# Kernel optimization log

Measured on AMD Instinct MI355X. Metric: run time of the kernel, lower is better.

Reference implementation:

```python
import jax, jax.numpy as jnp
import numpy as np

B, L = 16, 65536
NUM_BINS = 256
H = 64


def setup_inputs() -> dict:
    key = jax.random.key(0)
    k1, k2, k3, k4 = jax.random.split(key, 4)
    x = jax.random.normal(k1, (B, L), dtype=jnp.float32)
    mask = jax.random.uniform(k4, (B, L)) < 0.1
    x = jnp.where(mask, jnp.nan, x)
    # monotonically increasing bin edges
    bins = jnp.sort(jax.random.normal(k2, (NUM_BINS,), dtype=jnp.float32) * 1.5)
    # nn.Embedding(num_bins + 1, H), default init N(0,1); row 0 is the mask token
    emb_table = jax.random.normal(k3, (NUM_BINS + 1, H), dtype=jnp.float32)
    return {"x": x, "bins": bins, "emb_table": emb_table}


def reference(x, bins, emb_table):
    # BinEmbedding.bin with left_closed=True:
    #   idx = clamp(argmin([x>=b for b in bins] ++ [0]) - 1, min=0)
    # which equals clamp(count(bins <= x) - 1, min=0) = clamp(searchsorted(right) - 1, 0).
    # NaN inputs compare False everywhere in torch -> argmin=0 -> idx=0, then the
    # forward re-injects NaN and DiscreteEmbedding maps NaN -> token 0 (mask).
    nans = jnp.isnan(x)
    xs = jnp.where(nans, jnp.float32(0.0), x)  # sanitize for searchsorted
    idx = jnp.maximum(jnp.searchsorted(bins, xs, side="right") - 1, 0)  # (B, L)
    tok = jnp.where(nans, 0, idx + 1)  # +1 shift; 0 reserved for mask token
    return emb_table[tok]  # (B, L, H)
```

## Files before the change

kernel.cpp:

```cpp
#include <hip/hip_runtime.h>
#include <stdint.h>

#define N_POS (16 * 65536)
#define NBINS 256
#define HDIM  64


typedef float vfloat4 __attribute__((ext_vector_type(4)));

#define THREADS        256
#define POS_PER_TILE   256
#define TILES          8
#define POS_PER_BLOCK  (POS_PER_TILE * TILES)
#define NBLOCKS        (N_POS / POS_PER_BLOCK)
#define EMB_ROWS       (NBINS + 1)
#define EMB_CHUNKS     (EMB_ROWS * 16)

__global__ __launch_bounds__(THREADS, 2)
void BinEmbedding_49520972923592_kernel(
    const float* __restrict__ x,
    const float* __restrict__ bins,
    const vfloat4* __restrict__ embv,
    vfloat4* __restrict__ out)
{
    __shared__ vfloat4 s_emb[EMB_CHUNKS];
    __shared__ float   s_bins[NBINS];
    __shared__ int     s_tok[2][POS_PER_TILE];

    const int tid = threadIdx.x;

    s_bins[tid] = bins[tid];
    for (int c = tid; c < EMB_CHUNKS; c += THREADS)
        s_emb[c] = embv[c];

    const long pbase = (long)blockIdx.x * POS_PER_BLOCK;
    float xv = x[pbase + tid];
    __syncthreads();

    for (int tile = 0; tile < TILES; ++tile) {
        int cnt = 0;
#pragma unroll
        for (int step = 128; step >= 1; step >>= 1) {
            const int cand = cnt + step;
            cnt = (s_bins[cand - 1] <= xv) ? cand : cnt;
        }
        cnt += (s_bins[NBINS - 1] <= xv) ? 1 : 0;

        s_tok[tile & 1][tid] = (xv != xv) ? 0 : (cnt > 0 ? cnt : 1);

        if (tile + 1 < TILES)
            xv = x[pbase + (tile + 1) * POS_PER_TILE + tid];

        __syncthreads();

        const int* st = s_tok[tile & 1];
        const long cbase = (pbase + (long)tile * POS_PER_TILE) * 16;
#pragma unroll
        for (int i = 0; i < 16; ++i) {
            const int l = i * THREADS + tid;
            out[cbase + l] = s_emb[st[l >> 4] * 16 + (l & 15)];
        }
    }
}

extern "C" void kernel_launch(void* const* d_in, const int* in_sizes, int n_in,
                              void* d_out, int out_size, void* d_ws, size_t ws_size,
                              hipStream_t stream) {
    const float*   x    = (const float*)d_in[0];
    const float*   bins = (const float*)d_in[1];
    const vfloat4* emb  = (const vfloat4*)d_in[2];
    vfloat4* out = (vfloat4*)d_out;

    const dim3 grid(NBLOCKS), block(THREADS);
    hipLaunchKernelGGL(BinEmbedding_49520972923592_kernel, grid, block, 0, stream,
                       x, bins, emb, out);
}
```

Measured before the change: 271.9 us.

## Batch binary searches across all positions per thread before a single store phase

```diff
diff --git a/kernel.cpp b/kernel.cpp
--- a/kernel.cpp
+++ b/kernel.cpp
@@ -9,10 +9,10 @@
 typedef float vfloat4 __attribute__((ext_vector_type(4)));
 
 #define THREADS        256
-#define POS_PER_TILE   256
-#define TILES          8
-#define POS_PER_BLOCK  (POS_PER_TILE * TILES)
+#define POS_PER_TH     8
+#define POS_PER_BLOCK  (THREADS * POS_PER_TH)
 #define NBLOCKS        (N_POS / POS_PER_BLOCK)
+#define CHUNKS_PER_BLOCK (POS_PER_BLOCK * 16)
 #define EMB_ROWS       (NBINS + 1)
 #define EMB_CHUNKS     (EMB_ROWS * 16)
 
@@ -25,41 +25,49 @@
 {
     __shared__ vfloat4 s_emb[EMB_CHUNKS];
     __shared__ float   s_bins[NBINS];
-    __shared__ int     s_tok[2][POS_PER_TILE];
+    __shared__ int     s_tok[POS_PER_BLOCK];
 
     const int tid = threadIdx.x;
+    const long pbase = (long)blockIdx.x * POS_PER_BLOCK;
 
     s_bins[tid] = bins[tid];
-    for (int c = tid; c < EMB_CHUNKS; c += THREADS)
-        s_emb[c] = embv[c];
+#pragma unroll
+    for (int c = tid, k = 0; k < EMB_CHUNKS / THREADS + 1; ++k, c += THREADS)
+        if (c < EMB_CHUNKS) s_emb[c] = embv[c];
 
-    const long pbase = (long)blockIdx.x * POS_PER_BLOCK;
-    float xv = x[pbase + tid];
+    float xv[POS_PER_TH];
+#pragma unroll
+    for (int j = 0; j < POS_PER_TH; ++j)
+        xv[j] = x[pbase + j * THREADS + tid];
+
     __syncthreads();
 
-    for (int tile = 0; tile < TILES; ++tile) {
-        int cnt = 0;
+    int cnt[POS_PER_TH];
 #pragma unroll
-        for (int step = 128; step >= 1; step >>= 1) {
-            const int cand = cnt + step;
-            cnt = (s_bins[cand - 1] <= xv) ? cand : cnt;
+    for (int j = 0; j < POS_PER_TH; ++j) cnt[j] = 0;
+#pragma unroll
+    for (int step = 128; step >= 1; step >>= 1) {
+#pragma unroll
+        for (int j = 0; j < POS_PER_TH; ++j) {
+            const int cand = cnt[j] + step;
+            cnt[j] = (s_bins[cand - 1] <= xv[j]) ? cand : cnt[j];
         }
-        cnt += (s_bins[NBINS - 1] <= xv) ? 1 : 0;
+    }
+#pragma unroll
+    for (int j = 0; j < POS_PER_TH; ++j) {
+        const int c = cnt[j] + ((s_bins[NBINS - 1] <= xv[j]) ? 1 : 0);
+        s_tok[j * THREADS + tid] = (xv[j] != xv[j]) ? 0 : (c > 0 ? c : 1);
+    }
 
-        s_tok[tile & 1][tid] = (xv != xv) ? 0 : (cnt > 0 ? cnt : 1);
+    __syncthreads();
 
-        if (tile + 1 < TILES)
-            xv = x[pbase + (tile + 1) * POS_PER_TILE + tid];
-
-        __syncthreads();
-
-        const int* st = s_tok[tile & 1];
-        const long cbase = (pbase + (long)tile * POS_PER_TILE) * 16;
-#pragma unroll
-        for (int i = 0; i < 16; ++i) {
-            const int l = i * THREADS + tid;
-            out[cbase + l] = s_emb[st[l >> 4] * 16 + (l & 15)];
-        }
+    const long cbase = (long)blockIdx.x * CHUNKS_PER_BLOCK;
+    const int  c4    = tid & 15;
+    const int  g16   = tid >> 4;
+#pragma unroll 8
+    for (int k = 0; k < CHUNKS_PER_BLOCK / THREADS; ++k) {
+        const int tok = s_tok[k * (THREADS / 16) + g16];
+        out[cbase + k * THREADS + tid] = s_emb[tok * 16 + c4];
     }
 }
 
```

Result: faster. 264.4 us (-2.8%).
